# Kernel tuning notes

Measured on AMD Instinct MI355X. Metric: run time of the kernel, lower is better.

## Reference

```python
import jax, jax.numpy as jnp
import numpy as np

NUM_CLASSES = 256


def setup_inputs() -> dict:
    key = jax.random.key(0)
    k1, k2 = jax.random.split(key)
    B = 524288
    logits = jax.random.normal(k1, (B, NUM_CLASSES), dtype=jnp.float32)
    targets = jax.random.randint(k2, (B,), 0, NUM_CLASSES, dtype=jnp.int64)
    return {"logits": logits, "targets": targets}


def reference(logits, targets):
    # cumulative logits along class dim: (B, C)
    cum = jnp.cumsum(logits, axis=1)
    C = logits.shape[1]
    # only thresholds k in [0, C-2] contribute (original loops range(C-1))
    ks = jnp.arange(C - 1)  # (C-1,)
    cum = cum[:, : C - 1]  # (B, C-1)
    # if k < target: loss += -logsigmoid(-cum[k]); else: loss += -logsigmoid(cum[k])
    sign = jnp.where(ks[None, :] < targets[:, None], -1.0, 1.0)  # (B, C-1)
    per_elem = -jax.nn.log_sigmoid(sign * cum)
    per_sample = jnp.sum(per_elem, axis=1)  # (B,)
    return jnp.mean(per_sample)
```

## Files before the change

### kernel.cpp

```cpp
#include <hip/hip_runtime.h>
#include <hip/hip_bf16.h>


#define WAVE 64
#define BLOCK 256
#define WAVES_PER_BLOCK (BLOCK / WAVE)
#define NBLOCKS 8192
#define NCLASS 256

__device__ __forceinline__ float softplus_f(float z) {
    float az = fabsf(z);
    float e  = __expf(-az);
    return fmaxf(z, 0.0f) + __logf(1.0f + e);
}

__global__ __launch_bounds__(BLOCK) void ordloss_main(
        const float* __restrict__ logits,
        const int*   __restrict__ targets,
        double*      __restrict__ partials,
        int B, int rows_per_wave) {
    const int lane = threadIdx.x & (WAVE - 1);
    const int wib  = threadIdx.x >> 6;
    const long long waveGlobal = (long long)blockIdx.x * WAVES_PER_BLOCK + wib;
    const long long rowBase = waveGlobal * rows_per_wave;

    double acc = 0.0;

    for (int i = 0; i < rows_per_wave; ++i) {
        long long row = rowBase + i;
        if (row >= B) break;

        const float4 v = reinterpret_cast<const float4*>(logits + row * NCLASS)[lane];
        const int t = targets[row];

        float l0 = v.x;
        float l1 = l0 + v.y;
        float l2 = l1 + v.z;
        float l3 = l2 + v.w;
        const float tot = l3;

        float sc = tot;
        #pragma unroll
        for (int off = 1; off < WAVE; off <<= 1) {
            float y = __shfl_up(sc, off, WAVE);
            if (lane >= off) sc += y;
        }
        const float excl = sc - tot;

        const float c0 = excl + l0;
        const float c1 = excl + l1;
        const float c2 = excl + l2;
        const float c3 = excl + l3;

        const int k0 = lane << 2;
        float lsum;
        lsum  = softplus_f((k0 + 0 < t) ? c0 : -c0);
        lsum += softplus_f((k0 + 1 < t) ? c1 : -c1);
        lsum += softplus_f((k0 + 2 < t) ? c2 : -c2);
        if (lane < WAVE - 1)
            lsum += softplus_f((k0 + 3 < t) ? c3 : -c3);

        acc += (double)lsum;
    }

    #pragma unroll
    for (int off = 32; off > 0; off >>= 1)
        acc += __shfl_down(acc, off, WAVE);

    __shared__ double sdata[WAVES_PER_BLOCK];
    if (lane == 0) sdata[wib] = acc;
    __syncthreads();
    if (threadIdx.x == 0) {
        double s = 0.0;
        #pragma unroll
        for (int w = 0; w < WAVES_PER_BLOCK; ++w) s += sdata[w];
        partials[blockIdx.x] = s;
    }
}

__global__ __launch_bounds__(256) void ordloss_reduce(
        const double* __restrict__ partials, int n,
        float* __restrict__ out, double invB) {
    __shared__ double smem[256];
    double s = 0.0;
    for (int i = threadIdx.x; i < n; i += 256) s += partials[i];
    smem[threadIdx.x] = s;
    __syncthreads();
    for (int st = 128; st > 0; st >>= 1) {
        if (threadIdx.x < st) smem[threadIdx.x] += smem[threadIdx.x + st];
        __syncthreads();
    }
    if (threadIdx.x == 0) out[0] = (float)(smem[0] * invB);
}

extern "C" void kernel_launch(void* const* d_in, const int* in_sizes, int n_in,
                              void* d_out, int out_size, void* d_ws, size_t ws_size,
                              hipStream_t stream) {
    const float* logits  = (const float*)d_in[0];
    const int*   targets = (const int*)d_in[1];
    float*       out     = (float*)d_out;
    double*      partials = (double*)d_ws;

    const int B = in_sizes[1];
    const int total_waves = NBLOCKS * WAVES_PER_BLOCK;
    const int rows_per_wave = (B + total_waves - 1) / total_waves;

    ordloss_main<<<NBLOCKS, BLOCK, 0, stream>>>(logits, targets, partials, B, rows_per_wave);
    ordloss_reduce<<<1, 256, 0, stream>>>(partials, NBLOCKS, out, 1.0 / (double)B);
}
```

Measured before the change: 686.2 us.

## Rewrite ordinal loss with DPP scan, algebraic softplus split, and row prefetch

Replaces the shuffle-based wave scan with DPP row-shift/broadcast instructions. Softplus is decomposed as 0.5*(signed linear + |c|) plus a log term, and the four logs per lane are merged into one log of a product. Accumulation moves from double to float per lane. Each wave now processes a fixed 8 rows with a software prefetch of the next row, and the launch uses more blocks with an exact-size template specialisation. This cuts MUFU and shuffle work and hides load latency, at the cost of float accumulation precision and a fixed grid that changes the partials count.

```diff
diff --git a/kernel.cpp b/kernel.cpp
--- a/kernel.cpp
+++ b/kernel.cpp
@@ -4,76 +4,104 @@
 
 #define WAVE 64
 #define BLOCK 256
-#define WAVES_PER_BLOCK (BLOCK / WAVE)
-#define NBLOCKS 8192
+#define WPB (BLOCK / WAVE)
+#define ROWS 8
 #define NCLASS 256
 
-__device__ __forceinline__ float softplus_f(float z) {
-    float az = fabsf(z);
-    float e  = __expf(-az);
-    return fmaxf(z, 0.0f) + __logf(1.0f + e);
+__device__ __forceinline__ float wave_incl_scan(float s) {
+    int t;
+    t = __builtin_amdgcn_update_dpp(0, __float_as_int(s), 0x111, 0xf, 0xf, true); s += __int_as_float(t);
+    t = __builtin_amdgcn_update_dpp(0, __float_as_int(s), 0x112, 0xf, 0xf, true); s += __int_as_float(t);
+    t = __builtin_amdgcn_update_dpp(0, __float_as_int(s), 0x114, 0xf, 0xf, true); s += __int_as_float(t);
+    t = __builtin_amdgcn_update_dpp(0, __float_as_int(s), 0x118, 0xf, 0xf, true); s += __int_as_float(t);
+    t = __builtin_amdgcn_update_dpp(0, __float_as_int(s), 0x142, 0xa, 0xf, true); s += __int_as_float(t);
+    t = __builtin_amdgcn_update_dpp(0, __float_as_int(s), 0x143, 0xc, 0xf, true); s += __int_as_float(t);
+    return s;
 }
 
-__global__ __launch_bounds__(BLOCK) void ordloss_main(
+template <bool EXACT>
+__global__ __launch_bounds__(BLOCK, 4) void ordloss_main(
         const float* __restrict__ logits,
         const int*   __restrict__ targets,
         double*      __restrict__ partials,
-        int B, int rows_per_wave) {
+        int B) {
     const int lane = threadIdx.x & (WAVE - 1);
     const int wib  = threadIdx.x >> 6;
-    const long long waveGlobal = (long long)blockIdx.x * WAVES_PER_BLOCK + wib;
-    const long long rowBase = waveGlobal * rows_per_wave;
+    const long long rowBase = ((long long)blockIdx.x * WPB + wib) * ROWS;
+    const float lm = (lane == WAVE - 1) ? 0.0f : 1.0f;
+    const int k0 = lane << 2;
+    const float LOG2E = 1.4426950408889634f;
 
-    double acc = 0.0;
+    float acc_lin = 0.0f, acc_abs = 0.0f, acc_log = 0.0f;
 
-    for (int i = 0; i < rows_per_wave; ++i) {
-        long long row = rowBase + i;
-        if (row >= B) break;
+    const float4* p = reinterpret_cast<const float4*>(logits) + rowBase * (NCLASS / 4) + lane;
 
-        const float4 v = reinterpret_cast<const float4*>(logits + row * NCLASS)[lane];
-        const int t = targets[row];
+    float4 v = make_float4(0, 0, 0, 0);
+    int t = 0;
+    if (EXACT || rowBase < B) { v = p[0]; t = targets[rowBase]; }
 
-        float l0 = v.x;
-        float l1 = l0 + v.y;
-        float l2 = l1 + v.z;
-        float l3 = l2 + v.w;
-        const float tot = l3;
+    #pragma unroll
+    for (int i = 0; i < ROWS; ++i) {
+        const long long row = rowBase + i;
+        if (!EXACT && row >= B) break;
 
-        float sc = tot;
-        #pragma unroll
-        for (int off = 1; off < WAVE; off <<= 1) {
-            float y = __shfl_up(sc, off, WAVE);
-            if (lane >= off) sc += y;
+        float4 vn; int tn = 0;
+        if (i + 1 < ROWS) {
+            if (EXACT || row + 1 < B) { vn = p[(i + 1) * (NCLASS / 4)]; tn = targets[row + 1]; }
         }
-        const float excl = sc - tot;
+
+        const float l0 = v.x;
+        const float l1 = l0 + v.y;
+        const float l2 = l1 + v.z;
+        const float l3 = l2 + v.w;
+
+        const float incl = wave_incl_scan(l3);
+        const float excl = incl - l3;
 
         const float c0 = excl + l0;
         const float c1 = excl + l1;
         const float c2 = excl + l2;
         const float c3 = excl + l3;
 
-        const int k0 = lane << 2;
-        float lsum;
-        lsum  = softplus_f((k0 + 0 < t) ? c0 : -c0);
-        lsum += softplus_f((k0 + 1 < t) ? c1 : -c1);
-        lsum += softplus_f((k0 + 2 < t) ? c2 : -c2);
-        if (lane < WAVE - 1)
-            lsum += softplus_f((k0 + 3 < t) ? c3 : -c3);
+        const float a0 = fabsf(c0), a1 = fabsf(c1), a2 = fabsf(c2), a3 = fabsf(c3);
 
-        acc += (double)lsum;
+        const float u0 = __builtin_amdgcn_exp2f(-a0 * LOG2E);
+        const float u1 = __builtin_amdgcn_exp2f(-a1 * LOG2E);
+        const float u2 = __builtin_amdgcn_exp2f(-a2 * LOG2E);
+        const float u3 = __builtin_amdgcn_exp2f(-a3 * LOG2E) * lm;
+
+        float pr = 1.0f + u0;
+        pr = __builtin_fmaf(pr, u1, pr);
+        pr = __builtin_fmaf(pr, u2, pr);
+        pr = __builtin_fmaf(pr, u3, pr);
+        acc_log += __logf(pr);
+
+        const float c3m = c3 * lm;
+        acc_abs += a0 + a1 + a2 + a3 * lm;
+
+        const float sum_c = c0 + c1 + c2 + c3m;
+        float pre = 0.0f;
+        pre += (k0 + 0 < t) ? c0 : 0.0f;
+        pre += (k0 + 1 < t) ? c1 : 0.0f;
+        pre += (k0 + 2 < t) ? c2 : 0.0f;
+        pre += (k0 + 3 < t) ? c3 : 0.0f;
+        acc_lin += 2.0f * pre - sum_c;
+
+        v = vn; t = tn;
     }
 
+    double d = 0.5 * ((double)acc_lin + (double)acc_abs) + (double)acc_log;
     #pragma unroll
     for (int off = 32; off > 0; off >>= 1)
-        acc += __shfl_down(acc, off, WAVE);
+        d += __shfl_down(d, off, WAVE);
 
-    __shared__ double sdata[WAVES_PER_BLOCK];
-    if (lane == 0) sdata[wib] = acc;
+    __shared__ double sd[WPB];
+    if (lane == 0) sd[wib] = d;
     __syncthreads();
     if (threadIdx.x == 0) {
         double s = 0.0;
         #pragma unroll
-        for (int w = 0; w < WAVES_PER_BLOCK; ++w) s += sdata[w];
+        for (int w = 0; w < WPB; ++w) s += sd[w];
         partials[blockIdx.x] = s;
     }
 }
@@ -96,15 +124,19 @@
 extern "C" void kernel_launch(void* const* d_in, const int* in_sizes, int n_in,
                               void* d_out, int out_size, void* d_ws, size_t ws_size,
                               hipStream_t stream) {
-    const float* logits  = (const float*)d_in[0];
-    const int*   targets = (const int*)d_in[1];
-    float*       out     = (float*)d_out;
+    const float* logits   = (const float*)d_in[0];
+    const int*   targets  = (const int*)d_in[1];
+    float*       out      = (float*)d_out;
     double*      partials = (double*)d_ws;
 
     const int B = in_sizes[1];
-    const int total_waves = NBLOCKS * WAVES_PER_BLOCK;
-    const int rows_per_wave = (B + total_waves - 1) / total_waves;
+    const int rows_per_block = WPB * ROWS;
+    const int NB = (B + rows_per_block - 1) / rows_per_block;
 
-    ordloss_main<<<NBLOCKS, BLOCK, 0, stream>>>(logits, targets, partials, B, rows_per_wave);
-    ordloss_reduce<<<1, 256, 0, stream>>>(partials, NBLOCKS, out, 1.0 / (double)B);
+    if (B % rows_per_block == 0)
+        ordloss_main<true><<<NB, BLOCK, 0, stream>>>(logits, targets, partials, B);
+    else
+        ordloss_main<false><<<NB, BLOCK, 0, stream>>>(logits, targets, partials, B);
+
+    ordloss_reduce<<<1, 256, 0, stream>>>(partials, NB, out, 1.0 / (double)B);
 }
```

Result: no change. 690.2 us (+0.6%).
